# Optimization experiments

Hardware: AMD Instinct MI355X
Metric: run time of the kernel (lower is better)

The kernel has to match this reference:

```python
import jax, jax.numpy as jnp
import numpy as np

N_NODES = 100000
N_EDGES = 3200000
NODE_DIM = 128
HIDDEN = 16


def setup_inputs() -> dict:
    key = jax.random.key(0)
    ks = jax.random.split(key, 12)
    x = jax.random.normal(ks[0], (N_NODES, NODE_DIM), dtype=jnp.float32)
    edge_src = jax.random.randint(ks[1], (N_EDGES,), 0, N_NODES, dtype=jnp.int32)
    edge_dst = jax.random.randint(ks[2], (N_EDGES,), 0, N_NODES, dtype=jnp.int32)
    # QCNN block params (Linear(node_dim,16), Linear(16,16), Linear(16,16)) + classifier Linear(16,1)
    s1 = 1.0 / np.sqrt(NODE_DIM)
    s2 = 1.0 / np.sqrt(HIDDEN)
    W1 = jax.random.uniform(ks[3], (NODE_DIM, HIDDEN), jnp.float32, -s1, s1)
    b1 = jax.random.uniform(ks[4], (HIDDEN,), jnp.float32, -s1, s1)
    W2 = jax.random.uniform(ks[5], (HIDDEN, HIDDEN), jnp.float32, -s2, s2)
    b2 = jax.random.uniform(ks[6], (HIDDEN,), jnp.float32, -s2, s2)
    W3 = jax.random.uniform(ks[7], (HIDDEN, HIDDEN), jnp.float32, -s2, s2)
    b3 = jax.random.uniform(ks[8], (HIDDEN,), jnp.float32, -s2, s2)
    Wc = jax.random.uniform(ks[9], (HIDDEN, 1), jnp.float32, -s2, s2)
    bc = jax.random.uniform(ks[10], (1,), jnp.float32, -s2, s2)
    return {"x": x, "edge_src": edge_src, "edge_dst": edge_dst,
            "W1": W1, "b1": b1, "W2": W2, "b2": b2, "W3": W3, "b3": b3,
            "Wc": Wc, "bc": bc}


def reference(x, edge_src, edge_dst, W1, b1, W2, b2, W3, b3, Wc, bc):
    # per-node tiny 3-layer tanh MLP (QCNN block), vectorized over all nodes
    h = jnp.tanh(x @ W1 + b1)
    h = jnp.tanh(h @ W2 + b2)
    h = jnp.tanh(h @ W3 + b3)  # [N, H]
    n = x.shape[0]
    # degree of each aggregating node; nodes with no neighbors contribute 0
    deg = jnp.zeros((n,), x.dtype).at[edge_src].add(1.0)
    inv_deg = jnp.where(deg > 0, 1.0 / jnp.maximum(deg, 1.0), 0.0)
    # aggregated = sum_n mean_{m in N(n)} h[m] = sum_e h[dst_e] / deg[src_e]
    agg = jnp.sum(h[edge_dst] * inv_deg[edge_src][:, None], axis=0) / n  # [H]
    return jax.nn.sigmoid(agg @ Wc + bc)  # [1]
```

## Files before the change

kernel.cpp:

```cpp
#include <hip/hip_runtime.h>
#include <math.h>


#define NODE_DIM 128
#define HID 16

typedef __attribute__((ext_vector_type(8))) short    bfrag8;
typedef __attribute__((ext_vector_type(4))) _Float16 hfrag4;
typedef __attribute__((ext_vector_type(4))) float    f32x4;

__device__ __forceinline__ float fast_tanh(float x) {
    x = fminf(fmaxf(x, -10.0f), 10.0f);
    float e = __expf(2.0f * x);
    return (e - 1.0f) * __frcp_rn(e + 1.0f);
}
__device__ __forceinline__ unsigned short f2bf(float f) {
    unsigned u = __float_as_uint(f);
    return (unsigned short)((u + 0x7FFFu + ((u >> 16) & 1u)) >> 16);
}

__global__ __launch_bounds__(256) void k_mlp(
    const float* __restrict__ x,
    const float* __restrict__ W1, const float* __restrict__ b1,
    const float* __restrict__ W2, const float* __restrict__ b2,
    const float* __restrict__ W3, const float* __restrict__ b3,
    const float* __restrict__ Wc,
    unsigned char* __restrict__ c_code,
    float* __restrict__ gtotal, unsigned int* __restrict__ ticket,
    int n_nodes)
{
    if (blockIdx.x == 0 && threadIdx.x == 0) { *gtotal = 0.0f; *ticket = 0u; }

    const int lane = threadIdx.x & 63;
    const int col  = lane & 15;
    const int q    = lane >> 4;

    const int ngroups = (n_nodes + 15) >> 4;
    const int wgid    = (blockIdx.x * blockDim.x + threadIdx.x) >> 6;
    if (wgid >= ngroups) return;

    const int node0 = wgid << 4;
    int m = node0 + col;
    int mload = (m < n_nodes) ? m : (n_nodes - 1);
    const float* xr = x + (size_t)mload * NODE_DIM;

    float4 xa[4], xb[4];
#pragma unroll
    for (int kc = 0; kc < 4; ++kc) {
        const float* p = xr + kc * 32 + q * 8;
        xa[kc] = *reinterpret_cast<const float4*>(p);
        xb[kc] = *reinterpret_cast<const float4*>(p + 4);
    }

    bfrag8 w1f[4];
#pragma unroll
    for (int kc = 0; kc < 4; ++kc)
#pragma unroll
        for (int j = 0; j < 8; ++j)
            w1f[kc][j] = (short)f2bf(W1[(kc * 32 + q * 8 + j) * HID + col]);

    hfrag4 w2t, w3t;
#pragma unroll
    for (int j = 0; j < 4; ++j) {
        w2t[j] = (_Float16)W2[(q * 4 + j) * HID + col];
        w3t[j] = (_Float16)W3[(q * 4 + j) * HID + col];
    }
    float bb1[4], bb2[4], bb3[4], wcr[4];
#pragma unroll
    for (int j = 0; j < 4; ++j) {
        bb1[j] = b1[q * 4 + j]; bb2[j] = b2[q * 4 + j];
        bb3[j] = b3[q * 4 + j]; wcr[j] = Wc[q * 4 + j];
    }

    const f32x4 zero = {0.f, 0.f, 0.f, 0.f};
    f32x4 d1 = zero;
#pragma unroll
    for (int kc = 0; kc < 4; ++kc) {
        bfrag8 bf;
        bf[0] = (short)f2bf(xa[kc].x); bf[1] = (short)f2bf(xa[kc].y);
        bf[2] = (short)f2bf(xa[kc].z); bf[3] = (short)f2bf(xa[kc].w);
        bf[4] = (short)f2bf(xb[kc].x); bf[5] = (short)f2bf(xb[kc].y);
        bf[6] = (short)f2bf(xb[kc].z); bf[7] = (short)f2bf(xb[kc].w);
        d1 = __builtin_amdgcn_mfma_f32_16x16x32_bf16(w1f[kc], bf, d1, 0, 0, 0);
    }
    hfrag4 h1;
#pragma unroll
    for (int r = 0; r < 4; ++r) h1[r] = (_Float16)fast_tanh(d1[r] + bb1[r]);

    f32x4 d2 = __builtin_amdgcn_mfma_f32_16x16x16f16(w2t, h1, zero, 0, 0, 0);
    hfrag4 h2;
#pragma unroll
    for (int r = 0; r < 4; ++r) h2[r] = (_Float16)fast_tanh(d2[r] + bb2[r]);

    f32x4 d3 = __builtin_amdgcn_mfma_f32_16x16x16f16(w3t, h2, zero, 0, 0, 0);

    float v = 0.0f;
#pragma unroll
    for (int r = 0; r < 4; ++r) v += fast_tanh(d3[r] + bb3[r]) * wcr[r];
    v += __shfl_xor(v, 16, 64);
    v += __shfl_xor(v, 32, 64);

    if (lane < 16) {
        const int node = node0 + lane;
        if (node < n_nodes) {
            float c = fminf(fmaxf(v, -4.0f), 4.0f);
            c_code[node] = (unsigned char)__float2int_rn((c + 4.0f) * 16.0f);
        }
    }
}

__global__ __launch_bounds__(1024) void k_edge1(
    const int* __restrict__ src, const int* __restrict__ dst,
    const unsigned char* __restrict__ c_code,
    unsigned int* __restrict__ tables,
    int n_edges, int ch, int n_chunks, int n_slices, int code_bytes)
{
    extern __shared__ unsigned char dynlds[];
    unsigned char* scode = dynlds;
    unsigned int*  tab   = (unsigned int*)(dynlds + code_bytes);
    const int tid   = threadIdx.x;
    const int chunk = blockIdx.x % n_chunks;
    const int slice = blockIdx.x / n_chunks;
    const int lo    = chunk * ch;
    const int words = ch >> 1;

    const unsigned int* cp = reinterpret_cast<const unsigned int*>(c_code);
    unsigned int* scp = reinterpret_cast<unsigned int*>(scode);
    for (int i = tid; i < (code_bytes >> 2); i += 1024) scp[i] = cp[i];
    uint4* t4 = reinterpret_cast<uint4*>(tab);
    const uint4 z4 = {0u, 0u, 0u, 0u};
    for (int i = tid; i < (words >> 2); i += 1024) t4[i] = z4;
    __syncthreads();

    const int epb = ((n_edges + n_slices - 1) / n_slices + 7) & ~7;
    const int e0 = slice * epb;
    const int e1 = min(e0 + epb, n_edges);

    for (int e = e0 + (tid << 3); e < e1; e += 1024 * 8) {
        if (e + 7 < e1) {
            int4 s0 = *reinterpret_cast<const int4*>(src + e);
            int4 s1 = *reinterpret_cast<const int4*>(src + e + 4);
            int4 d0 = *reinterpret_cast<const int4*>(dst + e);
            int4 d1 = *reinterpret_cast<const int4*>(dst + e + 4);
            unsigned c0 = scode[d0.x], c1 = scode[d0.y];
            unsigned c2 = scode[d0.z], c3 = scode[d0.w];
            unsigned c4 = scode[d1.x], c5 = scode[d1.y];
            unsigned c6 = scode[d1.z], c7 = scode[d1.w];
            int i0 = s0.x - lo, i1 = s0.y - lo, i2 = s0.z - lo, i3 = s0.w - lo;
            int i4 = s1.x - lo, i5 = s1.y - lo, i6 = s1.z - lo, i7 = s1.w - lo;
            if ((unsigned)i0 < (unsigned)ch) atomicAdd(&tab[i0 >> 1], ((1u << 12) | c0) << ((i0 & 1) << 4));
            if ((unsigned)i1 < (unsigned)ch) atomicAdd(&tab[i1 >> 1], ((1u << 12) | c1) << ((i1 & 1) << 4));
            if ((unsigned)i2 < (unsigned)ch) atomicAdd(&tab[i2 >> 1], ((1u << 12) | c2) << ((i2 & 1) << 4));
            if ((unsigned)i3 < (unsigned)ch) atomicAdd(&tab[i3 >> 1], ((1u << 12) | c3) << ((i3 & 1) << 4));
            if ((unsigned)i4 < (unsigned)ch) atomicAdd(&tab[i4 >> 1], ((1u << 12) | c4) << ((i4 & 1) << 4));
            if ((unsigned)i5 < (unsigned)ch) atomicAdd(&tab[i5 >> 1], ((1u << 12) | c5) << ((i5 & 1) << 4));
            if ((unsigned)i6 < (unsigned)ch) atomicAdd(&tab[i6 >> 1], ((1u << 12) | c6) << ((i6 & 1) << 4));
            if ((unsigned)i7 < (unsigned)ch) atomicAdd(&tab[i7 >> 1], ((1u << 12) | c7) << ((i7 & 1) << 4));
        } else {
            for (int j = e; j < e1; ++j) {
                int ss = src[j] - lo;
                if ((unsigned)ss < (unsigned)ch)
                    atomicAdd(&tab[ss >> 1],
                              ((1u << 12) | (unsigned)scode[dst[j]]) << ((ss & 1) << 4));
            }
        }
    }
    __syncthreads();
    uint4* out4 = reinterpret_cast<uint4*>(tables + (size_t)(slice * n_chunks + chunk) * words);
    for (int i = tid; i < (words >> 2); i += 1024) out4[i] = t4[i];
}

__global__ __launch_bounds__(256) void k_totalfinal(
    const unsigned int* __restrict__ tables, const float* __restrict__ bc,
    float* __restrict__ out, float* __restrict__ gtotal,
    unsigned int* __restrict__ ticket,
    int n_chunks, int ch, int n_slices, float inv_n, int ntb)
{
    __shared__ float swave[4];
    const int wpc = ch >> 1;
    const int wg  = blockIdx.x * blockDim.x + threadIdx.x;
    const int chunk = wg / wpc, w = wg - chunk * wpc;
    const unsigned int stride = (unsigned int)(n_chunks * wpc);
    const unsigned int base0  = (unsigned int)(chunk * wpc + w);

    unsigned int sfix = 0, scnt = 0;
    for (int s = 0; s < n_slices; s += 8) {
        unsigned int v[8];
#pragma unroll
        for (int k = 0; k < 8; ++k)
            v[k] = tables[(size_t)(s + k) * stride + base0];
#pragma unroll
        for (int k = 0; k < 8; ++k) {
            sfix += v[k] & 0x0FFF0FFFu;
            scnt += (v[k] >> 12) & 0x000F000Fu;
        }
    }
    const unsigned int cnt_lo = scnt & 0xFFFFu, cnt_hi = scnt >> 16;
    const unsigned int fix_lo = sfix & 0xFFFFu, fix_hi = sfix >> 16;
    float contrib = 0.0f;
    if (cnt_lo > 0) contrib += (float)fix_lo / (16.0f * (float)cnt_lo) - 4.0f;
    if (cnt_hi > 0) contrib += (float)fix_hi / (16.0f * (float)cnt_hi) - 4.0f;

    for (int off = 32; off > 0; off >>= 1) contrib += __shfl_down(contrib, off, 64);
    if ((threadIdx.x & 63) == 0) swave[threadIdx.x >> 6] = contrib;
    __syncthreads();
    if (threadIdx.x == 0) {
        float part = swave[0] + swave[1] + swave[2] + swave[3];
        atomicAdd(gtotal, part);
        __threadfence();
        unsigned int t = atomicAdd(ticket, 1u);
        if (t == (unsigned int)(ntb - 1)) {
            __threadfence();
            float tot = atomicAdd(gtotal, 0.0f);
            float sv = tot * inv_n + bc[0];
            out[0] = 1.0f / (1.0f + __expf(-sv));
        }
    }
}

extern "C" void kernel_launch(void* const* d_in, const int* in_sizes, int n_in,
                              void* d_out, int out_size, void* d_ws, size_t ws_size,
                              hipStream_t stream) {
    const float* x   = (const float*)d_in[0];
    const int* esrc  = (const int*)d_in[1];
    const int* edst  = (const int*)d_in[2];
    const float* W1  = (const float*)d_in[3];
    const float* b1  = (const float*)d_in[4];
    const float* W2  = (const float*)d_in[5];
    const float* b2  = (const float*)d_in[6];
    const float* W3  = (const float*)d_in[7];
    const float* b3  = (const float*)d_in[8];
    const float* Wc  = (const float*)d_in[9];
    const float* bc  = (const float*)d_in[10];

    const int n_nodes = in_sizes[0] / NODE_DIM;
    const int n_edges = in_sizes[1];

    const int code_bytes = (n_nodes + 1023) & ~1023;

    int nch, nsl;
    if (hipFuncSetAttribute((const void*)k_edge1,
            hipFuncAttributeMaxDynamicSharedMemorySize, 163840) == hipSuccess) {
        nch = 4; nsl = 64;
    } else {
        (void)hipFuncSetAttribute((const void*)k_edge1,
            hipFuncAttributeMaxDynamicSharedMemorySize, 131072);
        nch = 8; nsl = 32;
    }
    const int ch    = code_bytes / nch;
    const int words = ch >> 1;
    const size_t lds_b = (size_t)code_bytes + (size_t)ch * 2;

    const size_t tab_b = (size_t)nsl * nch * words * 4;
    unsigned int* tables  = (unsigned int*)d_ws;
    float* gtotal         = (float*)((char*)d_ws + tab_b);
    unsigned int* ticket  = (unsigned int*)(gtotal + 1);
    unsigned char* c_code = (unsigned char*)d_ws + tab_b + 16;

    const int ngroups = (n_nodes + 15) >> 4;
    const int mlp_wg  = (ngroups + 3) >> 2;
    k_mlp<<<mlp_wg, 256, 0, stream>>>(x, W1, b1, W2, b2, W3, b3, Wc,
                                      c_code, gtotal, ticket, n_nodes);

    k_edge1<<<nch * nsl, 1024, lds_b, stream>>>(
        esrc, edst, c_code, tables, n_edges, ch, nch, nsl, code_bytes);

    const int ntb = (nch * words) / 256;
    k_totalfinal<<<ntb, 256, 0, stream>>>(
        tables, bc, (float*)d_out, gtotal, ticket,
        nch, ch, nsl, 1.0f / (float)n_nodes, ntb);
}
```

Before: 148.6 us.

## Fuse MLP, edge scatter and reduction into one cooperative kernel

Combines the three kernels into a single cooperative launch using grid-wide syncs between the MLP, edge-histogram and final reduction phases. The MLP phase becomes grid-stride over node groups, and the final sigmoid is computed by block 0 after a last grid sync instead of a ticket counter. This removes inter-kernel launch gaps and the ticket logic. In exchange, the MLP runs at one 1024-thread block per CU with lower occupancy, and grid syncs add their own cost. The previous multi-kernel path is kept as a fallback if the cooperative launch fails.

```diff
diff --git a/kernel.cpp b/kernel.cpp
--- a/kernel.cpp
+++ b/kernel.cpp
@@ -1,5 +1,8 @@
 #include <hip/hip_runtime.h>
+#include <hip/hip_cooperative_groups.h>
 #include <math.h>
+
+namespace cg = cooperative_groups;
 
 
 #define NODE_DIM 128
@@ -19,38 +22,19 @@
     return (unsigned short)((u + 0x7FFFu + ((u >> 16) & 1u)) >> 16);
 }
 
-__global__ __launch_bounds__(256) void k_mlp(
+
+__device__ __forceinline__ void mlp_phase(
     const float* __restrict__ x,
     const float* __restrict__ W1, const float* __restrict__ b1,
     const float* __restrict__ W2, const float* __restrict__ b2,
     const float* __restrict__ W3, const float* __restrict__ b3,
     const float* __restrict__ Wc,
-    unsigned char* __restrict__ c_code,
-    float* __restrict__ gtotal, unsigned int* __restrict__ ticket,
-    int n_nodes)
-{
-    if (blockIdx.x == 0 && threadIdx.x == 0) { *gtotal = 0.0f; *ticket = 0u; }
-
-    const int lane = threadIdx.x & 63;
-    const int col  = lane & 15;
-    const int q    = lane >> 4;
-
+    unsigned char* __restrict__ c_code, int n_nodes,
+    int wgid, int nwaves, int lane)
+{
+    const int col = lane & 15;
+    const int q   = lane >> 4;
     const int ngroups = (n_nodes + 15) >> 4;
-    const int wgid    = (blockIdx.x * blockDim.x + threadIdx.x) >> 6;
-    if (wgid >= ngroups) return;
-
-    const int node0 = wgid << 4;
-    int m = node0 + col;
-    int mload = (m < n_nodes) ? m : (n_nodes - 1);
-    const float* xr = x + (size_t)mload * NODE_DIM;
-
-    float4 xa[4], xb[4];
-#pragma unroll
-    for (int kc = 0; kc < 4; ++kc) {
-        const float* p = xr + kc * 32 + q * 8;
-        xa[kc] = *reinterpret_cast<const float4*>(p);
-        xb[kc] = *reinterpret_cast<const float4*>(p + 4);
-    }
 
     bfrag8 w1f[4];
 #pragma unroll
@@ -73,70 +57,83 @@
     }
 
     const f32x4 zero = {0.f, 0.f, 0.f, 0.f};
-    f32x4 d1 = zero;
-#pragma unroll
-    for (int kc = 0; kc < 4; ++kc) {
-        bfrag8 bf;
-        bf[0] = (short)f2bf(xa[kc].x); bf[1] = (short)f2bf(xa[kc].y);
-        bf[2] = (short)f2bf(xa[kc].z); bf[3] = (short)f2bf(xa[kc].w);
-        bf[4] = (short)f2bf(xb[kc].x); bf[5] = (short)f2bf(xb[kc].y);
-        bf[6] = (short)f2bf(xb[kc].z); bf[7] = (short)f2bf(xb[kc].w);
-        d1 = __builtin_amdgcn_mfma_f32_16x16x32_bf16(w1f[kc], bf, d1, 0, 0, 0);
-    }
-    hfrag4 h1;
-#pragma unroll
-    for (int r = 0; r < 4; ++r) h1[r] = (_Float16)fast_tanh(d1[r] + bb1[r]);
-
-    f32x4 d2 = __builtin_amdgcn_mfma_f32_16x16x16f16(w2t, h1, zero, 0, 0, 0);
-    hfrag4 h2;
-#pragma unroll
-    for (int r = 0; r < 4; ++r) h2[r] = (_Float16)fast_tanh(d2[r] + bb2[r]);
-
-    f32x4 d3 = __builtin_amdgcn_mfma_f32_16x16x16f16(w3t, h2, zero, 0, 0, 0);
-
-    float v = 0.0f;
-#pragma unroll
-    for (int r = 0; r < 4; ++r) v += fast_tanh(d3[r] + bb3[r]) * wcr[r];
-    v += __shfl_xor(v, 16, 64);
-    v += __shfl_xor(v, 32, 64);
-
-    if (lane < 16) {
-        const int node = node0 + lane;
-        if (node < n_nodes) {
-            float c = fminf(fmaxf(v, -4.0f), 4.0f);
-            c_code[node] = (unsigned char)__float2int_rn((c + 4.0f) * 16.0f);
-        }
-    }
-}
-
-__global__ __launch_bounds__(1024) void k_edge1(
+    for (int g = wgid; g < ngroups; g += nwaves) {
+        const int node0 = g << 4;
+        int m = node0 + col;
+        int mload = (m < n_nodes) ? m : (n_nodes - 1);
+        const float* xr = x + (size_t)mload * NODE_DIM;
+
+        float4 xa[4], xb[4];
+#pragma unroll
+        for (int kc = 0; kc < 4; ++kc) {
+            const float* p = xr + kc * 32 + q * 8;
+            xa[kc] = *reinterpret_cast<const float4*>(p);
+            xb[kc] = *reinterpret_cast<const float4*>(p + 4);
+        }
+        f32x4 d1 = zero;
+#pragma unroll
+        for (int kc = 0; kc < 4; ++kc) {
+            bfrag8 bf;
+            bf[0] = (short)f2bf(xa[kc].x); bf[1] = (short)f2bf(xa[kc].y);
+            bf[2] = (short)f2bf(xa[kc].z); bf[3] = (short)f2bf(xa[kc].w);
+            bf[4] = (short)f2bf(xb[kc].x); bf[5] = (short)f2bf(xb[kc].y);
+            bf[6] = (short)f2bf(xb[kc].z); bf[7] = (short)f2bf(xb[kc].w);
+            d1 = __builtin_amdgcn_mfma_f32_16x16x32_bf16(w1f[kc], bf, d1, 0, 0, 0);
+        }
+        hfrag4 h1;
+#pragma unroll
+        for (int r = 0; r < 4; ++r) h1[r] = (_Float16)fast_tanh(d1[r] + bb1[r]);
+
+        f32x4 d2 = __builtin_amdgcn_mfma_f32_16x16x16f16(w2t, h1, zero, 0, 0, 0);
+        hfrag4 h2;
+#pragma unroll
+        for (int r = 0; r < 4; ++r) h2[r] = (_Float16)fast_tanh(d2[r] + bb2[r]);
+
+        f32x4 d3 = __builtin_amdgcn_mfma_f32_16x16x16f16(w3t, h2, zero, 0, 0, 0);
+
+        float v = 0.0f;
+#pragma unroll
+        for (int r = 0; r < 4; ++r) v += fast_tanh(d3[r] + bb3[r]) * wcr[r];
+        v += __shfl_xor(v, 16, 64);
+        v += __shfl_xor(v, 32, 64);
+
+        if (lane < 16) {
+            const int node = node0 + lane;
+            if (node < n_nodes) {
+                float c = fminf(fmaxf(v, -4.0f), 4.0f);
+                c_code[node] = (unsigned char)__float2int_rn((c + 4.0f) * 16.0f);
+            }
+        }
+    }
+}
+
+__device__ __forceinline__ void edge_phase(
     const int* __restrict__ src, const int* __restrict__ dst,
     const unsigned char* __restrict__ c_code,
-    unsigned int* __restrict__ tables,
-    int n_edges, int ch, int n_chunks, int n_slices, int code_bytes)
-{
-    extern __shared__ unsigned char dynlds[];
+    unsigned int* __restrict__ tables, unsigned char* dynlds,
+    int n_edges, int ch, int n_chunks, int n_slices, int code_bytes,
+    int bid, int tid, int nthreads)
+{
     unsigned char* scode = dynlds;
     unsigned int*  tab   = (unsigned int*)(dynlds + code_bytes);
-    const int tid   = threadIdx.x;
-    const int chunk = blockIdx.x % n_chunks;
-    const int slice = blockIdx.x / n_chunks;
+    const int chunk = bid % n_chunks;
+    const int slice = bid / n_chunks;
     const int lo    = chunk * ch;
     const int words = ch >> 1;
 
     const unsigned int* cp = reinterpret_cast<const unsigned int*>(c_code);
     unsigned int* scp = reinterpret_cast<unsigned int*>(scode);
-    for (int i = tid; i < (code_bytes >> 2); i += 1024) scp[i] = cp[i];
+    for (int i = tid; i < (code_bytes >> 2); i += nthreads) scp[i] = cp[i];
     uint4* t4 = reinterpret_cast<uint4*>(tab);
     const uint4 z4 = {0u, 0u, 0u, 0u};
-    for (int i = tid; i < (words >> 2); i += 1024) t4[i] = z4;
+    for (int i = tid; i < (words >> 2); i += nthreads) t4[i] = z4;
     __syncthreads();
 
     const int epb = ((n_edges + n_slices - 1) / n_slices + 7) & ~7;
     const int e0 = slice * epb;
     const int e1 = min(e0 + epb, n_edges);
 
-    for (int e = e0 + (tid << 3); e < e1; e += 1024 * 8) {
+    for (int e = e0 + (tid << 3); e < e1; e += nthreads * 8) {
         if (e + 7 < e1) {
             int4 s0 = *reinterpret_cast<const int4*>(src + e);
             int4 s1 = *reinterpret_cast<const int4*>(src + e + 4);
@@ -167,7 +164,117 @@
     }
     __syncthreads();
     uint4* out4 = reinterpret_cast<uint4*>(tables + (size_t)(slice * n_chunks + chunk) * words);
-    for (int i = tid; i < (words >> 2); i += 1024) out4[i] = t4[i];
+    for (int i = tid; i < (words >> 2); i += nthreads) out4[i] = t4[i];
+}
+
+__device__ __forceinline__ float total_contrib(
+    const unsigned int* __restrict__ tables, int t, int words_total,
+    unsigned int stride, int n_slices)
+{
+    if (t >= words_total) return 0.0f;
+    unsigned int sfix = 0, scnt = 0;
+    for (int s = 0; s < n_slices; s += 8) {
+#pragma unroll
+        for (int k = 0; k < 8; ++k) {
+            unsigned int v = tables[(size_t)(s + k) * stride + (unsigned)t];
+            sfix += v & 0x0FFF0FFFu;
+            scnt += (v >> 12) & 0x000F000Fu;
+        }
+    }
+    const unsigned int cnt_lo = scnt & 0xFFFFu, cnt_hi = scnt >> 16;
+    const unsigned int fix_lo = sfix & 0xFFFFu, fix_hi = sfix >> 16;
+    float contrib = 0.0f;
+    if (cnt_lo > 0) contrib += (float)fix_lo / (16.0f * (float)cnt_lo) - 4.0f;
+    if (cnt_hi > 0) contrib += (float)fix_hi / (16.0f * (float)cnt_hi) - 4.0f;
+    return contrib;
+}
+
+__global__ __launch_bounds__(1024) void k_fused(
+    const float* __restrict__ x,
+    const int* __restrict__ src, const int* __restrict__ dst,
+    const float* __restrict__ W1, const float* __restrict__ b1,
+    const float* __restrict__ W2, const float* __restrict__ b2,
+    const float* __restrict__ W3, const float* __restrict__ b3,
+    const float* __restrict__ Wc, const float* __restrict__ bc,
+    unsigned char* __restrict__ c_code, unsigned int* __restrict__ tables,
+    float* __restrict__ gtotal, float* __restrict__ out,
+    int n_nodes, int n_edges, int ch, int nch, int nsl, int code_bytes,
+    float inv_n)
+{
+    extern __shared__ unsigned char dynlds[];
+    __shared__ float swave[16];
+    cg::grid_group grid = cg::this_grid();
+    const int tid = threadIdx.x;
+
+    if (blockIdx.x == 0 && tid == 0) *gtotal = 0.0f;
+
+    {
+        const int lane   = tid & 63;
+        const int nwaves = (gridDim.x * blockDim.x) >> 6;
+        const int wgid   = (blockIdx.x * blockDim.x + tid) >> 6;
+        mlp_phase(x, W1, b1, W2, b2, W3, b3, Wc, c_code, n_nodes,
+                  wgid, nwaves, lane);
+    }
+    __threadfence();
+    grid.sync();
+
+    edge_phase(src, dst, c_code, tables, dynlds,
+               n_edges, ch, nch, nsl, code_bytes, blockIdx.x, tid, 1024);
+    __threadfence();
+    grid.sync();
+
+    {
+        const int words       = ch >> 1;
+        const int words_total = nch * words;
+        const unsigned int stride = (unsigned int)words_total;
+        const int t = blockIdx.x * blockDim.x + tid;
+        float contrib = total_contrib(tables, t, words_total, stride, nsl);
+
+        for (int off = 32; off > 0; off >>= 1) contrib += __shfl_down(contrib, off, 64);
+        if ((tid & 63) == 0) swave[tid >> 6] = contrib;
+        __syncthreads();
+        if (tid == 0) {
+            float s = 0.0f;
+#pragma unroll
+            for (int w = 0; w < 16; ++w) s += swave[w];
+            atomicAdd(gtotal, s);
+            __threadfence();
+        }
+    }
+    grid.sync();
+    if (blockIdx.x == 0 && tid == 0) {
+        float sv = (*gtotal) * inv_n + bc[0];
+        out[0] = 1.0f / (1.0f + __expf(-sv));
+    }
+}
+
+__global__ __launch_bounds__(256) void k_mlp(
+    const float* __restrict__ x,
+    const float* __restrict__ W1, const float* __restrict__ b1,
+    const float* __restrict__ W2, const float* __restrict__ b2,
+    const float* __restrict__ W3, const float* __restrict__ b3,
+    const float* __restrict__ Wc,
+    unsigned char* __restrict__ c_code,
+    float* __restrict__ gtotal, unsigned int* __restrict__ ticket,
+    int n_nodes)
+{
+    if (blockIdx.x == 0 && threadIdx.x == 0) { *gtotal = 0.0f; *ticket = 0u; }
+    const int lane   = threadIdx.x & 63;
+    const int nwaves = (gridDim.x * blockDim.x) >> 6;
+    const int wgid   = (blockIdx.x * blockDim.x + threadIdx.x) >> 6;
+    mlp_phase(x, W1, b1, W2, b2, W3, b3, Wc, c_code, n_nodes, wgid, nwaves, lane);
+}
+
+__global__ __launch_bounds__(1024) void k_edge1(
+    const int* __restrict__ src, const int* __restrict__ dst,
+    const unsigned char* __restrict__ c_code,
+    unsigned int* __restrict__ tables,
+    int n_edges, int ch, int n_chunks, int n_slices, int code_bytes)
+{
+    extern __shared__ unsigned char dynlds[];
+    edge_phase(src, dst, c_code, tables, dynlds,
+               n_edges, ch, n_chunks, n_slices, code_bytes,
+               blockIdx.x, threadIdx.x, 1024);
 }
 
 __global__ __launch_bounds__(256) void k_totalfinal(
@@ -177,29 +284,11 @@
     int n_chunks, int ch, int n_slices, float inv_n, int ntb)
 {
     __shared__ float swave[4];
-    const int wpc = ch >> 1;
-    const int wg  = blockIdx.x * blockDim.x + threadIdx.x;
-    const int chunk = wg / wpc, w = wg - chunk * wpc;
-    const unsigned int stride = (unsigned int)(n_chunks * wpc);
-    const unsigned int base0  = (unsigned int)(chunk * wpc + w);
-
-    unsigned int sfix = 0, scnt = 0;
-    for (int s = 0; s < n_slices; s += 8) {
-        unsigned int v[8];
-#pragma unroll
-        for (int k = 0; k < 8; ++k)
-            v[k] = tables[(size_t)(s + k) * stride + base0];
-#pragma unroll
-        for (int k = 0; k < 8; ++k) {
-            sfix += v[k] & 0x0FFF0FFFu;
-            scnt += (v[k] >> 12) & 0x000F000Fu;
-        }
-    }
-    const unsigned int cnt_lo = scnt & 0xFFFFu, cnt_hi = scnt >> 16;
-    const unsigned int fix_lo = sfix & 0xFFFFu, fix_hi = sfix >> 16;
-    float contrib = 0.0f;
-    if (cnt_lo > 0) contrib += (float)fix_lo / (16.0f * (float)cnt_lo) - 4.0f;
-    if (cnt_hi > 0) contrib += (float)fix_hi / (16.0f * (float)cnt_hi) - 4.0f;
+    const int words       = ch >> 1;
+    const int words_total = n_chunks * words;
+    const int t = blockIdx.x * blockDim.x + threadIdx.x;
+    float contrib = total_contrib(tables, t, words_total,
+                                  (unsigned int)words_total, n_slices);
 
     for (int off = 32; off > 0; off >>= 1) contrib += __shfl_down(contrib, off, 64);
     if ((threadIdx.x & 63) == 0) swave[threadIdx.x >> 6] = contrib;
@@ -208,8 +297,8 @@
         float part = swave[0] + swave[1] + swave[2] + swave[3];
         atomicAdd(gtotal, part);
         __threadfence();
-        unsigned int t = atomicAdd(ticket, 1u);
-        if (t == (unsigned int)(ntb - 1)) {
+        unsigned int tk = atomicAdd(ticket, 1u);
+        if (tk == (unsigned int)(ntb - 1)) {
             __threadfence();
             float tot = atomicAdd(gtotal, 0.0f);
             float sv = tot * inv_n + bc[0];
@@ -235,15 +324,14 @@
 
     const int n_nodes = in_sizes[0] / NODE_DIM;
     const int n_edges = in_sizes[1];
-
     const int code_bytes = (n_nodes + 1023) & ~1023;
 
     int nch, nsl;
-    if (hipFuncSetAttribute((const void*)k_edge1,
+    if (hipFuncSetAttribute((const void*)k_fused,
             hipFuncAttributeMaxDynamicSharedMemorySize, 163840) == hipSuccess) {
         nch = 4; nsl = 64;
     } else {
-        (void)hipFuncSetAttribute((const void*)k_edge1,
+        (void)hipFuncSetAttribute((const void*)k_fused,
             hipFuncAttributeMaxDynamicSharedMemorySize, 131072);
         nch = 8; nsl = 32;
     }
@@ -256,17 +344,38 @@
     float* gtotal         = (float*)((char*)d_ws + tab_b);
     unsigned int* ticket  = (unsigned int*)(gtotal + 1);
     unsigned char* c_code = (unsigned char*)d_ws + tab_b + 16;
-
+    float* outp           = (float*)d_out;
+    float inv_n           = 1.0f / (float)n_nodes;
+
+    {
+        int nch_a = nch, nsl_a = nsl, ch_a = ch, cb_a = code_bytes;
+        int nn = n_nodes, ne = n_edges;
+        void* args[] = {
+            (void*)&x, (void*)&esrc, (void*)&edst,
+            (void*)&W1, (void*)&b1, (void*)&W2, (void*)&b2,
+            (void*)&W3, (void*)&b3, (void*)&Wc, (void*)&bc,
+            (void*)&c_code, (void*)&tables, (void*)&gtotal, (void*)&outp,
+            (void*)&nn, (void*)&ne, (void*)&ch_a, (void*)&nch_a,
+            (void*)&nsl_a, (void*)&cb_a, (void*)&inv_n };
+        hipError_t err = hipLaunchCooperativeKernel(
+            (const void*)k_fused, dim3(nch * nsl), dim3(1024),
+            args, (unsigned int)lds_b, stream);
+        if (err == hipSuccess) return;
+        (void)hipGetLastError();
+    }
+
+    if (hipFuncSetAttribute((const void*)k_edge1,
+            hipFuncAttributeMaxDynamicSharedMemorySize, 163840) != hipSuccess) {
+        (void)hipFuncSetAttribute((const void*)k_edge1,
+            hipFuncAttributeMaxDynamicSharedMemorySize, 131072);
+    }
     const int ngroups = (n_nodes + 15) >> 4;
     const int mlp_wg  = (ngroups + 3) >> 2;
     k_mlp<<<mlp_wg, 256, 0, stream>>>(x, W1, b1, W2, b2, W3, b3, Wc,
                                       c_code, gtotal, ticket, n_nodes);
-
     k_edge1<<<nch * nsl, 1024, lds_b, stream>>>(
         esrc, edst, c_code, tables, n_edges, ch, nch, nsl, code_bytes);
-
     const int ntb = (nch * words) / 256;
     k_totalfinal<<<ntb, 256, 0, stream>>>(
-        tables, bc, (float*)d_out, gtotal, ticket,
-        nch, ch, nsl, 1.0f / (float)n_nodes, ntb);
-}
+        tables, bc, outp, gtotal, ticket, nch, ch, nsl, inv_n, ntb);
+}
```

Result: slower. 495.2 us (+233.2%).
